# Performance work log

Hardware: AMD Instinct MI355X
Metric: run time of the kernel (lower is better)

The kernel has to match this reference:

```python
import jax, jax.numpy as jnp
import numpy as np

EPS = 1e-08


def setup_inputs() -> dict:
    key = jax.random.key(0)
    k1, k2, k3 = jax.random.split(key, 3)
    B, C, D, H, W = 2, 4, 128, 192, 192
    net_output = jax.random.normal(k1, (B, C, D, H, W), dtype=jnp.float32)
    target = jax.random.randint(k2, (B, 1, D, H, W), 0, C, dtype=jnp.int64)
    dist = jax.random.uniform(k3, (B, D, H, W), dtype=jnp.float32)
    return {"net_output": net_output, "target": target, "dist": dist}


def reference(net_output, target, dist):
    # net_output: [B, C, D, H, W]; target: [B, 1, D, H, W] int; dist: [B, D, H, W]
    B, C = net_output.shape[0], net_output.shape[1]
    # one-hot scatter along channel dim (scatter_(1, target, 1))
    cls = jnp.arange(C, dtype=target.dtype).reshape((1, C) + (1,) * (net_output.ndim - 2))
    y_onehot = (target == cls).astype(net_output.dtype)  # [B, C, D, H, W]

    # channels i >= 1: overlay dist, then per-(b, i)-slice min-max normalize
    z = y_onehot[:, 1:] * dist[:, None]  # [B, C-1, D, H, W]
    spatial_axes = tuple(range(2, z.ndim))
    mn = jnp.min(z, axis=spatial_axes, keepdims=True)
    mx = jnp.max(z, axis=spatial_axes, keepdims=True)
    zn = (z - mn) / (mx + EPS - mn)
    dist_y = jnp.concatenate([y_onehot[:, :1], zn], axis=1)  # [B, C, D, H, W]
    dist_y = jax.lax.stop_gradient(dist_y)  # built under no_grad / from non-grad leaves

    # CrossEntropyLoss with soft (probability) targets: mean over batch+spatial
    logp = jax.nn.log_softmax(net_output, axis=1)
    loss = -(dist_y * logp).sum(axis=1).mean()
    return loss
```

## Files before the change

kernel.cpp:

```cpp
#include <hip/hip_runtime.h>

#define NB 2
#define NS (128 * 192 * 192)
#define NTOT (NB * NS)
#define NSQ (NS / 4)
#define EPSF 1e-8f
#define INF_BITS 0x7F800000u

#define TPB 256
#define BPB 768
#define BLOCKS (2 * BPB)
#define STRIDE (BPB * TPB)
#define ITERS (NSQ / STRIDE)



typedef float __attribute__((ext_vector_type(4))) f32x4;
typedef int   __attribute__((ext_vector_type(4))) i32x4;

__device__ __forceinline__ f32x4 ldnt_f4(const float* p) {
    return __builtin_nontemporal_load((const f32x4*)p);
}
__device__ __forceinline__ i32x4 ldnt_i4(const int* p) {
    return __builtin_nontemporal_load((const i32x4*)p);
}

__global__ __launch_bounds__(TPB)
__attribute__((amdgpu_waves_per_eu(2, 6)))
void k_fused(const float* __restrict__ x,
             const int* __restrict__ tgt,
             const float* __restrict__ dist,
             float* __restrict__ part) {
    const int b = (blockIdx.x >= BPB) ? 1 : 0;
    const int bid = blockIdx.x - b * BPB;
    const int q0 = bid * TPB + threadIdx.x;

    const float* xb = x + (size_t)b * 4 * NSQ * 4;
    const int*   tb = tgt + (size_t)b * NSQ * 4;
    const float* db = dist + (size_t)b * NSQ * 4;

    float mn1 = __uint_as_float(INF_BITS), mn2 = mn1, mn3 = mn1;
    float mx1 = 0.f, mx2 = 0.f, mx3 = 0.f;
    float P1 = 0.f, P2 = 0.f, P3 = 0.f;
    float Q1 = 0.f, Q2 = 0.f, Q3 = 0.f;
    float R0 = 0.f;

    auto vox = [&](float a0, float a1, float a2, float a3, int tt, float dv) {
        float m = fmaxf(fmaxf(a0, a1), fmaxf(a2, a3));
        float e = __expf(a0 - m) + __expf(a1 - m) + __expf(a2 - m) + __expf(a3 - m);
        float lse = m + __logf(e);
        float z1 = (tt == 1) ? dv : 0.f;
        float z2 = (tt == 2) ? dv : 0.f;
        float z3 = (tt == 3) ? dv : 0.f;
        mn1 = fminf(mn1, z1); mx1 = fmaxf(mx1, z1);
        mn2 = fminf(mn2, z2); mx2 = fmaxf(mx2, z2);
        mn3 = fminf(mn3, z3); mx3 = fmaxf(mx3, z3);
        float l1 = a1 - lse, l2 = a2 - lse, l3 = a3 - lse;
        P1 += z1 * l1; P2 += z2 * l2; P3 += z3 * l3;
        Q1 += l1; Q2 += l2; Q3 += l3;
        R0 += (tt == 0) ? (a0 - lse) : 0.f;
    };

    f32x4 cx0 = ldnt_f4(xb + (size_t)q0 * 4);
    f32x4 cx1 = ldnt_f4(xb + (size_t)(q0 + NSQ) * 4);
    f32x4 cx2 = ldnt_f4(xb + (size_t)(q0 + 2 * NSQ) * 4);
    f32x4 cx3 = ldnt_f4(xb + (size_t)(q0 + 3 * NSQ) * 4);
    i32x4 ct  = ldnt_i4(tb + (size_t)q0 * 4);
    f32x4 cd  = ldnt_f4(db + (size_t)q0 * 4);

#pragma unroll 1
    for (int i = 0; i < ITERS; i++) {
        f32x4 nx0, nx1, nx2, nx3, nd;
        i32x4 nt;
        if (i + 1 < ITERS) {
            const int qn = q0 + (i + 1) * STRIDE;
            nx0 = ldnt_f4(xb + (size_t)qn * 4);
            nx1 = ldnt_f4(xb + (size_t)(qn + NSQ) * 4);
            nx2 = ldnt_f4(xb + (size_t)(qn + 2 * NSQ) * 4);
            nx3 = ldnt_f4(xb + (size_t)(qn + 3 * NSQ) * 4);
            nt  = ldnt_i4(tb + (size_t)qn * 4);
            nd  = ldnt_f4(db + (size_t)qn * 4);
        }
        vox(cx0.x, cx1.x, cx2.x, cx3.x, ct.x, cd.x);
        vox(cx0.y, cx1.y, cx2.y, cx3.y, ct.y, cd.y);
        vox(cx0.z, cx1.z, cx2.z, cx3.z, ct.z, cd.z);
        vox(cx0.w, cx1.w, cx2.w, cx3.w, ct.w, cd.w);
        if (i + 1 < ITERS) {
            cx0 = nx0; cx1 = nx1; cx2 = nx2; cx3 = nx3; ct = nt; cd = nd;
        }
    }

    for (int off = 32; off; off >>= 1) {
        mn1 = fminf(mn1, __shfl_down(mn1, off, 64));
        mn2 = fminf(mn2, __shfl_down(mn2, off, 64));
        mn3 = fminf(mn3, __shfl_down(mn3, off, 64));
        mx1 = fmaxf(mx1, __shfl_down(mx1, off, 64));
        mx2 = fmaxf(mx2, __shfl_down(mx2, off, 64));
        mx3 = fmaxf(mx3, __shfl_down(mx3, off, 64));
        P1 += __shfl_down(P1, off, 64);
        P2 += __shfl_down(P2, off, 64);
        P3 += __shfl_down(P3, off, 64);
        Q1 += __shfl_down(Q1, off, 64);
        Q2 += __shfl_down(Q2, off, 64);
        Q3 += __shfl_down(Q3, off, 64);
        R0 += __shfl_down(R0, off, 64);
    }

    __shared__ float sv[4][13];
    const int wid = threadIdx.x >> 6;
    if ((threadIdx.x & 63) == 0) {
        sv[wid][0] = mn1; sv[wid][1] = mn2; sv[wid][2] = mn3;
        sv[wid][3] = mx1; sv[wid][4] = mx2; sv[wid][5] = mx3;
        sv[wid][6] = P1;  sv[wid][7] = P2;  sv[wid][8] = P3;
        sv[wid][9] = Q1;  sv[wid][10] = Q2; sv[wid][11] = Q3;
        sv[wid][12] = R0;
    }
    __syncthreads();
    const int i = threadIdx.x;
    if (i < 13) {
        float v = sv[0][i];
        if (i < 3)      v = fminf(fminf(v, sv[1][i]), fminf(sv[2][i], sv[3][i]));
        else if (i < 6) v = fmaxf(fmaxf(v, sv[1][i]), fmaxf(sv[2][i], sv[3][i]));
        else            v = v + sv[1][i] + sv[2][i] + sv[3][i];
        part[(size_t)blockIdx.x * 16 + i] = v;
    }
}

__global__ __launch_bounds__(512, 1)
void k_final(const float* __restrict__ part, float* __restrict__ out) {
    const int t = threadIdx.x;
    const int batch = t >> 8;
    const int lane8 = t & 255;

    float mn[3] = {__uint_as_float(INF_BITS), __uint_as_float(INF_BITS), __uint_as_float(INF_BITS)};
    float mx[3] = {0.f, 0.f, 0.f};
    double P[3] = {0, 0, 0}, Q[3] = {0, 0, 0}, R0 = 0;

#pragma unroll
    for (int k = 0; k < 3; k++) {
        const float4* r = (const float4*)(part + (size_t)(batch * BPB + k * 256 + lane8) * 16);
        float4 r0 = r[0];
        float4 r1 = r[1];
        float4 r2 = r[2];
        float4 r3 = r[3];
        mn[0] = fminf(mn[0], r0.x); mn[1] = fminf(mn[1], r0.y); mn[2] = fminf(mn[2], r0.z);
        mx[0] = fmaxf(mx[0], r0.w); mx[1] = fmaxf(mx[1], r1.x); mx[2] = fmaxf(mx[2], r1.y);
        P[0] += (double)r1.z; P[1] += (double)r1.w; P[2] += (double)r2.x;
        Q[0] += (double)r2.y; Q[1] += (double)r2.z; Q[2] += (double)r2.w;
        R0 += (double)r3.x;
    }

    for (int off = 32; off; off >>= 1) {
#pragma unroll
        for (int j = 0; j < 3; j++) {
            mn[j] = fminf(mn[j], __shfl_down(mn[j], off, 64));
            mx[j] = fmaxf(mx[j], __shfl_down(mx[j], off, 64));
            P[j] += __shfl_down(P[j], off, 64);
            Q[j] += __shfl_down(Q[j], off, 64);
        }
        R0 += __shfl_down(R0, off, 64);
    }

    __shared__ float smn[8][3], smx[8][3];
    __shared__ double sP[8][3], sQ[8][3], sR[8];
    const int wid = t >> 6;
    if ((t & 63) == 0) {
#pragma unroll
        for (int j = 0; j < 3; j++) {
            smn[wid][j] = mn[j]; smx[wid][j] = mx[j];
            sP[wid][j] = P[j];   sQ[wid][j] = Q[j];
        }
        sR[wid] = R0;
    }
    __syncthreads();
    if (t == 0) {
        double acc = 0.0;
#pragma unroll
        for (int b = 0; b < 2; b++) {
            double Pb[3] = {0, 0, 0}, Qb[3] = {0, 0, 0};
            float mnb[3], mxb[3];
#pragma unroll
            for (int j = 0; j < 3; j++) { mnb[j] = __uint_as_float(INF_BITS); mxb[j] = 0.f; }
#pragma unroll
            for (int w = 4 * b; w < 4 * b + 4; w++) {
                acc += sR[w];
#pragma unroll
                for (int j = 0; j < 3; j++) {
                    mnb[j] = fminf(mnb[j], smn[w][j]);
                    mxb[j] = fmaxf(mxb[j], smx[w][j]);
                    Pb[j] += sP[w][j];
                    Qb[j] += sQ[w][j];
                }
            }
#pragma unroll
            for (int j = 0; j < 3; j++) {
                float sf = 1.0f / (mxb[j] + EPSF - mnb[j]);
                acc += (double)sf * (Pb[j] - (double)mnb[j] * Qb[j]);
            }
        }
        out[0] = (float)(-acc / (double)NTOT);
    }
}

extern "C" void kernel_launch(void* const* d_in, const int* in_sizes, int n_in,
                              void* d_out, int out_size, void* d_ws, size_t ws_size,
                              hipStream_t stream) {
    const float* net = (const float*)d_in[0];
    const int* tgt = (const int*)d_in[1];
    const float* dist = (const float*)d_in[2];
    float* part = (float*)d_ws;

    k_fused<<<BLOCKS, TPB, 0, stream>>>(net, tgt, dist, part);
    k_final<<<1, 512, 0, stream>>>(part, (float*)d_out);
}
```

Measured before the change: 247.7 us.

## Stream inputs through LDS via global_load_lds double buffering

Replaces the register-prefetched nontemporal vector loads with direct global-to-LDS loads (global_load_lds, 16 bytes per lane). Each wave double-buffers a 6 KB slice and uses explicit waitcnt and a sched_barrier to overlap the next tile's loads with compute on the current one. The waves_per_eu attribute is dropped. The intent is to cut register pressure and keep more bytes in flight for this bandwidth-bound reduction, at the cost of 48 KB of LDS per block, which may limit occupancy, plus extra LDS read traffic.

```diff
diff --git a/kernel.cpp b/kernel.cpp
--- a/kernel.cpp
+++ b/kernel.cpp
@@ -14,19 +14,16 @@
 #define ITERS (NSQ / STRIDE)
 
 
-
 typedef float __attribute__((ext_vector_type(4))) f32x4;
 typedef int   __attribute__((ext_vector_type(4))) i32x4;
 
-__device__ __forceinline__ f32x4 ldnt_f4(const float* p) {
-    return __builtin_nontemporal_load((const f32x4*)p);
-}
-__device__ __forceinline__ i32x4 ldnt_i4(const int* p) {
-    return __builtin_nontemporal_load((const i32x4*)p);
+__device__ __forceinline__ void gld_lds16(const void* g, void* l) {
+    __builtin_amdgcn_global_load_lds(
+        (const __attribute__((address_space(1))) void*)g,
+        (__attribute__((address_space(3))) void*)l, 16, 0, 0);
 }
 
 __global__ __launch_bounds__(TPB)
-__attribute__((amdgpu_waves_per_eu(2, 6)))
 void k_fused(const float* __restrict__ x,
              const int* __restrict__ tgt,
              const float* __restrict__ dist,
@@ -34,10 +31,15 @@
     const int b = (blockIdx.x >= BPB) ? 1 : 0;
     const int bid = blockIdx.x - b * BPB;
     const int q0 = bid * TPB + threadIdx.x;
-
-    const float* xb = x + (size_t)b * 4 * NSQ * 4;
-    const int*   tb = tgt + (size_t)b * NSQ * 4;
-    const float* db = dist + (size_t)b * NSQ * 4;
+    const int wid = threadIdx.x >> 6;
+    const int lane = threadIdx.x & 63;
+
+    const char* xb = (const char*)x + (size_t)b * NSQ * 64;
+    const char* tb = (const char*)tgt + (size_t)b * NSQ * 16;
+    const char* db = (const char*)dist + (size_t)b * NSQ * 16;
+
+    __shared__ char sm[4 * 2 * 6 * 1024];
+    char* wb0 = sm + wid * 12288;
 
     float mn1 = __uint_as_float(INF_BITS), mn2 = mn1, mn3 = mn1;
     float mx1 = 0.f, mx2 = 0.f, mx3 = 0.f;
@@ -61,33 +63,44 @@
         R0 += (tt == 0) ? (a0 - lse) : 0.f;
     };
 
-    f32x4 cx0 = ldnt_f4(xb + (size_t)q0 * 4);
-    f32x4 cx1 = ldnt_f4(xb + (size_t)(q0 + NSQ) * 4);
-    f32x4 cx2 = ldnt_f4(xb + (size_t)(q0 + 2 * NSQ) * 4);
-    f32x4 cx3 = ldnt_f4(xb + (size_t)(q0 + 3 * NSQ) * 4);
-    i32x4 ct  = ldnt_i4(tb + (size_t)q0 * 4);
-    f32x4 cd  = ldnt_f4(db + (size_t)q0 * 4);
-
+    auto issue = [&](int i, int k) {
+        const size_t o = (size_t)(q0 + i * STRIDE) * 16;
+        char* lb = wb0 + k * 6144;
+        gld_lds16(xb + o,                     lb);
+        gld_lds16(xb + o + (size_t)NSQ * 16,  lb + 1024);
+        gld_lds16(xb + o + (size_t)NSQ * 32,  lb + 2048);
+        gld_lds16(xb + o + (size_t)NSQ * 48,  lb + 3072);
+        gld_lds16(tb + o,                     lb + 4096);
+        gld_lds16(db + o,                     lb + 5120);
+    };
+
+    auto consume = [&](int k) {
+        const char* lb = wb0 + k * 6144 + lane * 16;
+        f32x4 x0 = *(const f32x4*)(lb);
+        f32x4 x1 = *(const f32x4*)(lb + 1024);
+        f32x4 x2 = *(const f32x4*)(lb + 2048);
+        f32x4 x3 = *(const f32x4*)(lb + 3072);
+        i32x4 tt = *(const i32x4*)(lb + 4096);
+        f32x4 dd = *(const f32x4*)(lb + 5120);
+        vox(x0.x, x1.x, x2.x, x3.x, tt.x, dd.x);
+        vox(x0.y, x1.y, x2.y, x3.y, tt.y, dd.y);
+        vox(x0.z, x1.z, x2.z, x3.z, tt.z, dd.z);
+        vox(x0.w, x1.w, x2.w, x3.w, tt.w, dd.w);
+    };
+
+    issue(0, 0);
 #pragma unroll 1
     for (int i = 0; i < ITERS; i++) {
-        f32x4 nx0, nx1, nx2, nx3, nd;
-        i32x4 nt;
+        const int cur = i & 1;
         if (i + 1 < ITERS) {
-            const int qn = q0 + (i + 1) * STRIDE;
-            nx0 = ldnt_f4(xb + (size_t)qn * 4);
-            nx1 = ldnt_f4(xb + (size_t)(qn + NSQ) * 4);
-            nx2 = ldnt_f4(xb + (size_t)(qn + 2 * NSQ) * 4);
-            nx3 = ldnt_f4(xb + (size_t)(qn + 3 * NSQ) * 4);
-            nt  = ldnt_i4(tb + (size_t)qn * 4);
-            nd  = ldnt_f4(db + (size_t)qn * 4);
-        }
-        vox(cx0.x, cx1.x, cx2.x, cx3.x, ct.x, cd.x);
-        vox(cx0.y, cx1.y, cx2.y, cx3.y, ct.y, cd.y);
-        vox(cx0.z, cx1.z, cx2.z, cx3.z, ct.z, cd.z);
-        vox(cx0.w, cx1.w, cx2.w, cx3.w, ct.w, cd.w);
-        if (i + 1 < ITERS) {
-            cx0 = nx0; cx1 = nx1; cx2 = nx2; cx3 = nx3; ct = nt; cd = nd;
-        }
+            asm volatile("s_waitcnt lgkmcnt(0)" ::: "memory");
+            issue(i + 1, cur ^ 1);
+            asm volatile("s_waitcnt vmcnt(6)" ::: "memory");
+        } else {
+            asm volatile("s_waitcnt vmcnt(0)" ::: "memory");
+        }
+        __builtin_amdgcn_sched_barrier(0);
+        consume(cur);
     }
 
     for (int off = 32; off; off >>= 1) {
@@ -107,7 +120,6 @@
     }
 
     __shared__ float sv[4][13];
-    const int wid = threadIdx.x >> 6;
     if ((threadIdx.x & 63) == 0) {
         sv[wid][0] = mn1; sv[wid][1] = mn2; sv[wid][2] = mn3;
         sv[wid][3] = mx1; sv[wid][4] = mx2; sv[wid][5] = mx3;
```

Measured after the change: 266.1 us. 1.07x slower.
